# Kernel optimization log

Measured on AMD Instinct MI355X. Metric: run time of the kernel, lower is better.

The kernel has to match this reference:

```python
import jax, jax.numpy as jnp
import numpy as np

IN_SIZE = 171
HIDDEN = 1024
OUT_SIZE = 171
BATCH = 64
SEQ_LEN = 100
COND_NUM = 5
GT_NUM = 5


def _lstm_cell(x, h, c, w_ih, w_hh, b_ih, b_hh):
    # PyTorch LSTMCell: gates ordered (i, f, g, o)
    gates = x @ w_ih.T + h @ w_hh.T + b_ih + b_hh  # [B, 4H]
    i, f, g, o = jnp.split(gates, 4, axis=-1)
    i = jax.nn.sigmoid(i)
    f = jax.nn.sigmoid(f)
    g = jnp.tanh(g)
    o = jax.nn.sigmoid(o)
    c_new = f * c + i * g
    h_new = o * jnp.tanh(c_new)
    return h_new, c_new


def setup_inputs() -> dict:
    key = jax.random.key(0)
    ks = jax.random.split(key, 15)
    s = 1.0 / np.sqrt(HIDDEN)
    p = {}
    p["real_seq"] = jax.random.normal(ks[0], (BATCH, SEQ_LEN, IN_SIZE), dtype=jnp.float32)
    p["w_ih1"] = jax.random.uniform(ks[1], (4 * HIDDEN, IN_SIZE), minval=-s, maxval=s, dtype=jnp.float32)
    p["w_hh1"] = jax.random.uniform(ks[2], (4 * HIDDEN, HIDDEN), minval=-s, maxval=s, dtype=jnp.float32)
    p["b_ih1"] = jax.random.uniform(ks[3], (4 * HIDDEN,), minval=-s, maxval=s, dtype=jnp.float32)
    p["b_hh1"] = jax.random.uniform(ks[4], (4 * HIDDEN,), minval=-s, maxval=s, dtype=jnp.float32)
    p["w_ih2"] = jax.random.uniform(ks[5], (4 * HIDDEN, HIDDEN), minval=-s, maxval=s, dtype=jnp.float32)
    p["w_hh2"] = jax.random.uniform(ks[6], (4 * HIDDEN, HIDDEN), minval=-s, maxval=s, dtype=jnp.float32)
    p["b_ih2"] = jax.random.uniform(ks[7], (4 * HIDDEN,), minval=-s, maxval=s, dtype=jnp.float32)
    p["b_hh2"] = jax.random.uniform(ks[8], (4 * HIDDEN,), minval=-s, maxval=s, dtype=jnp.float32)
    p["w_ih3"] = jax.random.uniform(ks[9], (4 * HIDDEN, HIDDEN), minval=-s, maxval=s, dtype=jnp.float32)
    p["w_hh3"] = jax.random.uniform(ks[10], (4 * HIDDEN, HIDDEN), minval=-s, maxval=s, dtype=jnp.float32)
    p["b_ih3"] = jax.random.uniform(ks[11], (4 * HIDDEN,), minval=-s, maxval=s, dtype=jnp.float32)
    p["b_hh3"] = jax.random.uniform(ks[12], (4 * HIDDEN,), minval=-s, maxval=s, dtype=jnp.float32)
    p["dec_w"] = jax.random.uniform(ks[13], (OUT_SIZE, HIDDEN), minval=-s, maxval=s, dtype=jnp.float32)
    p["dec_b"] = jax.random.uniform(ks[14], (OUT_SIZE,), minval=-s, maxval=s, dtype=jnp.float32)
    return p


def _condition_lst(seq_len):
    gt = np.ones((100, GT_NUM))
    cond = np.zeros((100, COND_NUM))
    return np.concatenate((gt, cond), axis=1).reshape(-1)[:seq_len]


def reference(real_seq, w_ih1, w_hh1, b_ih1, b_hh1, w_ih2, w_hh2, b_ih2, b_hh2,
              w_ih3, w_hh3, b_ih3, b_hh3, dec_w, dec_b):
    batch, seq_len, _ = real_seq.shape
    cond = jnp.asarray(_condition_lst(seq_len), dtype=real_seq.dtype)  # [T], static pattern
    frames = jnp.swapaxes(real_seq, 0, 1)  # [T, B, in]
    z = jnp.zeros((batch, HIDDEN), dtype=real_seq.dtype)
    out0 = jnp.zeros((batch, OUT_SIZE), dtype=real_seq.dtype)

    def step(carry, xs):
        (h0, c0, h1, c1, h2, c2, prev_out) = carry
        frame, c = xs
        in_frame = jnp.where(c == 1, frame, prev_out)
        h0, c0 = _lstm_cell(in_frame, h0, c0, w_ih1, w_hh1, b_ih1, b_hh1)
        h1, c1 = _lstm_cell(h0, h1, c1, w_ih2, w_hh2, b_ih2, b_hh2)
        h2, c2 = _lstm_cell(h1, h2, c2, w_ih3, w_hh3, b_ih3, b_hh3)
        out = h2 @ dec_w.T + dec_b
        return (h0, c0, h1, c1, h2, c2, out), out

    _, outs = jax.lax.scan(step, (z, z, z, z, z, z, out0), (frames, cond))  # outs [T, B, out]
    # torch concatenates along dim=1 -> [B, T*out]
    return jnp.swapaxes(outs, 0, 1).reshape(batch, seq_len * OUT_SIZE)
```

## Files before the change

### kernel.cpp

```cpp
#include <hip/hip_runtime.h>
#include <hip/hip_fp16.h>


typedef unsigned short u16;
typedef unsigned int u32;
typedef _Float16 f16;
typedef _Float16 h8 __attribute__((ext_vector_type(8)));
typedef float f4 __attribute__((ext_vector_type(4)));

#define HSZ 65536

static __device__ __forceinline__ f4 mfma16(h8 a, h8 b, f4 c) {
  return __builtin_amdgcn_mfma_f32_16x16x32_f16(a, b, c, 0, 0, 0);
}

static __device__ __forceinline__ float fsig(float x) {
  return 1.f / (1.f + __expf(-x));
}
static __device__ __forceinline__ float ftanh(float x) {
  return 1.f - 2.f / (1.f + __expf(2.f * x));
}

struct P {
  const u16 *w1h, *weff, *w1x, *w2, *w3, *wdec, *fr;
  const float *br, *ba, *b2s, *b3s, *dec_b;
  u16 *h0, *h1, *h2;
  float* out;
  u32* bar;
};

template<int NJ>
static __device__ __forceinline__ void gemm_hreg(f4* acc, const u16* __restrict__ h,
                                                 const h8 (&wr)[NJ], int kq, int bt2,
                                                 int q, int c) {
#pragma unroll
  for (int jj = 0; jj < NJ; ++jj) {
    int kt = kq * 8 + jj;
    const u16* hp = h + (size_t)(kt * 4 + q) * 512;
    h8 b = wr[jj];
#pragma unroll
    for (int t = 0; t < 2; ++t) {
      h8 a = *(const h8*)(hp + ((bt2 * 2 + t) * 16 + c) * 8);
      acc[t] = mfma16(a, b, acc[t]);
    }
  }
}

static __device__ __forceinline__ void gemm_hlds(f4* acc, const u16* __restrict__ h,
                                                 const u16* lw, int ktbase, int kq,
                                                 int bt2, int q, int c, int lane) {
#pragma unroll
  for (int jj = 0; jj < 8; ++jj) {
    int kt = kq * 8 + jj;
    h8 b = *(const h8*)(lw + (size_t)((ktbase + kt) * 64 + lane) * 8);
    const u16* hp = h + (size_t)(kt * 4 + q) * 512;
#pragma unroll
    for (int t = 0; t < 2; ++t) {
      h8 a = *(const h8*)(hp + ((bt2 * 2 + t) * 16 + c) * 8);
      acc[t] = mfma16(a, b, acc[t]);
    }
  }
}

static __device__ __forceinline__ void gemm_fr(f4* acc, const u16* __restrict__ frt,
                                               const h8 (&wr)[2], int kq, int bt2,
                                               int q, int c) {
  if (kq < 3) {
#pragma unroll
    for (int jj = 0; jj < 2; ++jj) {
      int kt = kq * 2 + jj;
      h8 b = wr[jj];
#pragma unroll
      for (int t = 0; t < 2; ++t) {
        h8 a = *(const h8*)(frt + (size_t)((bt2 * 2 + t) * 16 + c) * 192 + kt * 32 + q * 8);
        acc[t] = mfma16(a, b, acc[t]);
      }
    }
  }
}

__launch_bounds__(512, 2)
__global__ void lstm_main(P p) {
  const int ng = blockIdx.x;
  const int tid = threadIdx.x;
  const int lane = tid & 63;
  const int w = tid >> 6;
  const int kq = w & 3;
  const int bt2 = w >> 2;
  const int c = lane & 15;
  const int q = lane >> 4;

  __shared__ u16 lds_w2[64 * 512];
  __shared__ u16 lds_w3[64 * 512];
  __shared__ float part[4 * 64 * 17];
  __shared__ float decp[8][64];

  {
    const uint4* s2 = (const uint4*)(p.w2 + (size_t)ng * 64 * 512);
    const uint4* s3 = (const uint4*)(p.w3 + (size_t)ng * 64 * 512);
    uint4* d2 = (uint4*)lds_w2;
    uint4* d3 = (uint4*)lds_w3;
    for (int i = tid; i < 4096; i += 512) { d2[i] = s2[i]; d3[i] = s3[i]; }
  }

  h8 r_w1h[8], r_weff[8], r_w1x[2];
  {
#pragma unroll
    for (int jj = 0; jj < 8; ++jj) {
      r_w1h[jj] = *(const h8*)(p.w1h + (size_t)((ng * 32 + kq * 8 + jj) * 64 + lane) * 8);
      r_weff[jj] = *(const h8*)(p.weff + (size_t)((ng * 32 + kq * 8 + jj) * 64 + lane) * 8);
    }
    if (kq < 3) {
#pragma unroll
      for (int jj = 0; jj < 2; ++jj)
        r_w1x[jj] = *(const h8*)(p.w1x + (size_t)((ng * 6 + kq * 2 + jj) * 64 + lane) * 8);
    }
  }

  float rb_r[16], rb_a[16], rb2[16], rb3[16];
  if (w == 0) {
#pragma unroll
    for (int i = 0; i < 16; ++i) {
      int idx = (i >> 2) * 1024 + ng * 4 + (i & 3);
      rb_r[i] = p.br[idx];  rb_a[i] = p.ba[idx];
      rb2[i] = p.b2s[idx];  rb3[i] = p.b3s[idx];
    }
  }
  const float dec_bng = (ng < 171) ? p.dec_b[ng] : 0.f;
  __syncthreads();

  float cr0[4] = {0, 0, 0, 0}, cr1[4] = {0, 0, 0, 0}, cr2[4] = {0, 0, 0, 0};
  u32 pub = 0;

  auto combine_pub = [&](float* crL, const float* rb, u16* hw) {
    u32 pk0 = 0, pk1 = 0;
#pragma unroll
    for (int u = 0; u < 4; ++u) {
      float s0 = rb[0 + u], s1 = rb[4 + u], s2 = rb[8 + u], s3 = rb[12 + u];
#pragma unroll
      for (int kqi = 0; kqi < 4; ++kqi) {
        const float* pp = &part[(kqi * 64 + lane) * 17 + u];
        s0 += pp[0]; s1 += pp[4]; s2 += pp[8]; s3 += pp[12];
      }
      float iv = fsig(s0), fv = fsig(s1), gv = ftanh(s2), ov = fsig(s3);
      float cn = fv * crL[u] + iv * gv;
      crL[u] = cn;
      f16 hh = (f16)(ov * ftanh(cn));
      u32 bits = (u32)*(const u16*)&hh;
      if (u < 2) pk0 |= bits << (16 * u); else pk1 |= bits << (16 * (u - 2));
    }
    u32* dst = (u32*)hw + (size_t)(ng >> 1) * 256 + lane * 4 + (ng & 1) * 2;
    __hip_atomic_store(dst, pk0, __ATOMIC_RELAXED, __HIP_MEMORY_SCOPE_AGENT);
    __hip_atomic_store(dst + 1, pk1, __ATOMIC_RELAXED, __HIP_MEMORY_SCOPE_AGENT);
    __builtin_amdgcn_s_waitcnt(0x0f70);
    if (lane == 0)
      __hip_atomic_store(p.bar + ng, pub, __ATOMIC_RELAXED, __HIP_MEMORY_SCOPE_AGENT);
  };

  auto waitall = [&]() {
    if (w == 0) {
      for (;;) {
        u32 v0 = __hip_atomic_load(p.bar + lane, __ATOMIC_RELAXED, __HIP_MEMORY_SCOPE_AGENT);
        u32 v1 = __hip_atomic_load(p.bar + 64 + lane, __ATOMIC_RELAXED, __HIP_MEMORY_SCOPE_AGENT);
        u32 v2 = __hip_atomic_load(p.bar + 128 + lane, __ATOMIC_RELAXED, __HIP_MEMORY_SCOPE_AGENT);
        u32 v3 = __hip_atomic_load(p.bar + 192 + lane, __ATOMIC_RELAXED, __HIP_MEMORY_SCOPE_AGENT);
        u32 m01 = v0 < v1 ? v0 : v1;
        u32 m23 = v2 < v3 ? v2 : v3;
        u32 mn = m01 < m23 ? m01 : m23;
        if (__all((int)(mn >= pub))) break;
      }
    }
    __syncthreads();
  };

  auto put_part = [&](const f4* acc) {
#pragma unroll
    for (int t = 0; t < 2; ++t)
#pragma unroll
      for (int r = 0; r < 4; ++r)
        part[(kq * 64 + bt2 * 32 + t * 16 + q * 4 + r) * 17 + c] = acc[t][r];
  };

  auto dec_partial = [&](const u16* __restrict__ h2b) {
    if (ng < 171) {
      const u16* hp = h2b + (size_t)w * 16 * 512 + lane * 8;
      const u16* wp = p.wdec + (size_t)ng * 1024 + w * 128;
      float s = 0.f;
#pragma unroll 4
      for (int i = 0; i < 16; ++i) {
        h8 hv = *(const h8*)(hp + (size_t)i * 512);
        h8 wv8 = *(const h8*)(wp + i * 8);
#pragma unroll
        for (int jj = 0; jj < 8; ++jj) s += (float)hv[jj] * (float)wv8[jj];
      }
      decp[w][lane] = s;
    }
  };
  auto dec_reduce = [&](int tout) {
    if (ng < 171) {
      float o = dec_bng;
#pragma unroll
      for (int i = 0; i < 8; ++i) o += decp[i][lane];
      p.out[(size_t)lane * 17100 + (size_t)tout * 171 + ng] = o;
    }
  };

  for (int t = 0; t < 100; ++t) {
    const bool cond = (t % 10) < 5;
    const u16* h0r = p.h0 + (size_t)t * HSZ;
    const u16* h1r = p.h1 + (size_t)t * HSZ;
    const u16* h2r = p.h2 + (size_t)t * HSZ;
    u16* h0w = p.h0 + (size_t)(t + 1) * HSZ;
    u16* h1w = p.h1 + (size_t)(t + 1) * HSZ;
    u16* h2w = p.h2 + (size_t)(t + 1) * HSZ;

    {
      f4 acc[2] = {{0, 0, 0, 0}, {0, 0, 0, 0}};
      gemm_hreg<8>(acc, h0r, r_w1h, kq, bt2, q, c);
      if (cond) {
        gemm_fr(acc, p.fr + (size_t)t * 64 * 192, r_w1x, kq, bt2, q, c);
        __syncthreads();
      } else {
        waitall();
        gemm_hreg<8>(acc, h2r, r_weff, kq, bt2, q, c);
      }
      put_part(acc);
      __syncthreads();
      ++pub;
      if (w == 0) combine_pub(cr0, cond ? rb_r : rb_a, h0w);
    }
    {
      f4 acc[2] = {{0, 0, 0, 0}, {0, 0, 0, 0}};
      gemm_hlds(acc, h1r, lds_w2, 32, kq, bt2, q, c, lane);
      waitall();
      gemm_hlds(acc, h0w, lds_w2, 0, kq, bt2, q, c, lane);
      put_part(acc);
      __syncthreads();
      ++pub;
      if (w == 0) combine_pub(cr1, rb2, h1w);
    }
    {
      f4 acc[2] = {{0, 0, 0, 0}, {0, 0, 0, 0}};
      gemm_hlds(acc, h2r, lds_w3, 32, kq, bt2, q, c, lane);
      if (t > 0) dec_partial(h2r);
      waitall();
      gemm_hlds(acc, h1w, lds_w3, 0, kq, bt2, q, c, lane);
      put_part(acc);
      __syncthreads();
      ++pub;
      if (w == 0) combine_pub(cr2, rb3, h2w);
      else if (w == 1 && t > 0) dec_reduce(t - 1);
    }
  }
  waitall();
  dec_partial(p.h2 + (size_t)100 * HSZ);
  __syncthreads();
  if (w == 0) dec_reduce(99);
}


__global__ void pack_w_kernel(const float* __restrict__ srcA, int KA,
                              const float* __restrict__ srcB, int KB,
                              u16* __restrict__ dst, int nkt) {
  int blk = blockIdx.x;
  int ng = blk / nkt, kt = blk % nkt;
  int lane = threadIdx.x;
  int c = lane & 15, q = lane >> 4;
  int row = (c >> 2) * 1024 + ng * 4 + (c & 3);
  int k0 = kt * 32 + q * 8;
  alignas(16) u16 outv[8];
  for (int j = 0; j < 8; ++j) {
    int k = k0 + j;
    float v = 0.f;
    if (k < KA) v = srcA[(size_t)row * KA + k];
    else if (k - KA < KB) v = srcB[(size_t)row * KB + (k - KA)];
    f16 hv = (f16)v;
    outv[j] = *(u16*)&hv;
  }
  *(uint4*)(dst + ((size_t)blk * 64 + lane) * 8) = *(const uint4*)outv;
}

__global__ void pack_weff_kernel(const float* __restrict__ w_ih1,
                                 const float* __restrict__ dec_w, u16* __restrict__ dst) {
  int blk = blockIdx.x;
  int ng = blk >> 5, kt = blk & 31;
  int lane = threadIdx.x;
  int c = lane & 15, q = lane >> 4;
  int row = (c >> 2) * 1024 + ng * 4 + (c & 3);
  int k0 = kt * 32 + q * 8;
  float acc[8] = {0.f, 0.f, 0.f, 0.f, 0.f, 0.f, 0.f, 0.f};
  for (int r = 0; r < 171; ++r) {
    float wi = w_ih1[(size_t)row * 171 + r];
    const float* dw = dec_w + (size_t)r * 1024 + k0;
#pragma unroll
    for (int j = 0; j < 8; ++j) acc[j] += wi * dw[j];
  }
  alignas(16) u16 outv[8];
  for (int j = 0; j < 8; ++j) { f16 hv = (f16)acc[j]; outv[j] = *(u16*)&hv; }
  *(uint4*)(dst + ((size_t)blk * 64 + lane) * 8) = *(const uint4*)outv;
}

__global__ void prep_bias_kernel(const float* b_ih1, const float* b_hh1,
                                 const float* w_ih1, const float* dec_b,
                                 const float* b_ih2, const float* b_hh2,
                                 const float* b_ih3, const float* b_hh3,
                                 float* br, float* ba, float* b2, float* b3) {
  int n = blockIdx.x * 256 + threadIdx.x;
  float s = b_ih1[n] + b_hh1[n];
  br[n] = s;
  float a = 0.f;
  for (int r = 0; r < 171; ++r) a += w_ih1[(size_t)n * 171 + r] * dec_b[r];
  ba[n] = s + a;
  b2[n] = b_ih2[n] + b_hh2[n];
  b3[n] = b_ih3[n] + b_hh3[n];
}

__global__ void pack_frames_kernel(const float* __restrict__ rs, u16* __restrict__ fr) {
  int i = blockIdx.x * 256 + threadIdx.x;
  int j = i % 192;
  int tb = i / 192;
  int b = tb % 64, t = tb / 64;
  float v = (j < 171) ? rs[((size_t)b * 100 + t) * 171 + j] : 0.f;
  f16 hv = (f16)v;
  fr[i] = *(u16*)&hv;
}

__global__ void pack_wdec_kernel(const float* __restrict__ dw, u16* __restrict__ dst) {
  int i = blockIdx.x * 256 + threadIdx.x;
  if (i < 171 * 1024) { f16 hv = (f16)dw[i]; dst[i] = *(u16*)&hv; }
}

__global__ void zero_kernel(u32* h0, u32* h1, u32* h2, u32* bar) {
  int i = blockIdx.x * 256 + threadIdx.x;
  h0[i] = 0; h1[i] = 0; h2[i] = 0;
  if (blockIdx.x < 8) bar[i] = 0;
}

extern "C" void kernel_launch(void* const* d_in, const int* in_sizes, int n_in,
                              void* d_out, int out_size, void* d_ws, size_t ws_size,
                              hipStream_t stream) {
  const float* real_seq = (const float*)d_in[0];
  const float* w_ih1 = (const float*)d_in[1];
  const float* w_hh1 = (const float*)d_in[2];
  const float* b_ih1 = (const float*)d_in[3];
  const float* b_hh1 = (const float*)d_in[4];
  const float* w_ih2 = (const float*)d_in[5];
  const float* w_hh2 = (const float*)d_in[6];
  const float* b_ih2 = (const float*)d_in[7];
  const float* b_hh2 = (const float*)d_in[8];
  const float* w_ih3 = (const float*)d_in[9];
  const float* w_hh3 = (const float*)d_in[10];
  const float* b_ih3 = (const float*)d_in[11];
  const float* b_hh3 = (const float*)d_in[12];
  const float* dec_w = (const float*)d_in[13];
  const float* dec_b = (const float*)d_in[14];

  char* ws = (char*)d_ws;
  size_t off = 0;
  auto alloc = [&](size_t bytes) {
    char* pp = ws + off;
    off += (bytes + 255) & ~(size_t)255;
    return pp;
  };
  u16* w1h  = (u16*)alloc(256ULL * 32 * 512 * 2);
  u16* weff = (u16*)alloc(256ULL * 32 * 512 * 2);
  u16* w1x  = (u16*)alloc(256ULL * 6 * 512 * 2);
  u16* w2   = (u16*)alloc(256ULL * 64 * 512 * 2);
  u16* w3   = (u16*)alloc(256ULL * 64 * 512 * 2);
  u16* wdec = (u16*)alloc(171ULL * 1024 * 2);
  u16* fr   = (u16*)alloc(100ULL * 64 * 192 * 2);
  u16* h0   = (u16*)alloc(101ULL * HSZ * 2);
  u16* h1   = (u16*)alloc(101ULL * HSZ * 2);
  u16* h2   = (u16*)alloc(101ULL * HSZ * 2);
  float* br  = (float*)alloc(4096 * 4);
  float* ba  = (float*)alloc(4096 * 4);
  float* b2s = (float*)alloc(4096 * 4);
  float* b3s = (float*)alloc(4096 * 4);
  u32* bar   = (u32*)alloc(8192);
  (void)ws_size; (void)in_sizes; (void)n_in; (void)out_size;

  pack_w_kernel<<<256 * 32, 64, 0, stream>>>(w_hh1, 1024, nullptr, 0, w1h, 32);
  pack_w_kernel<<<256 * 6, 64, 0, stream>>>(w_ih1, 171, nullptr, 0, w1x, 6);
  pack_w_kernel<<<256 * 64, 64, 0, stream>>>(w_ih2, 1024, w_hh2, 1024, w2, 64);
  pack_w_kernel<<<256 * 64, 64, 0, stream>>>(w_ih3, 1024, w_hh3, 1024, w3, 64);
  pack_weff_kernel<<<256 * 32, 64, 0, stream>>>(w_ih1, dec_w, weff);
  pack_wdec_kernel<<<(171 * 1024 + 255) / 256, 256, 0, stream>>>(dec_w, wdec);
  pack_frames_kernel<<<100 * 64 * 192 / 256, 256, 0, stream>>>(real_seq, fr);
  prep_bias_kernel<<<16, 256, 0, stream>>>(b_ih1, b_hh1, w_ih1, dec_b,
                                           b_ih2, b_hh2, b_ih3, b_hh3, br, ba, b2s, b3s);
  zero_kernel<<<128, 256, 0, stream>>>((u32*)h0, (u32*)h1, (u32*)h2, bar);

  P p{w1h, weff, w1x, w2, w3, wdec, fr, br, ba, b2s, b3s, dec_b,
      h0, h1, h2, (float*)d_out, bar};
  lstm_main<<<256, 512, 0, stream>>>(p);
}
```

Measured before the change: 2.031 ms.

## Swap MFMA operands so each lane owns full gate quartets, replace LDS reduction with flag handoff

Each MFMA now takes the weight tile as the A operand and hidden state as B, so every lane ends up with all four gates (i,f,g,o) for one hidden unit. The K dimension is split into two halves instead of four, and the two partial sums are combined through a per-wave LDS flag handoff instead of block-wide __syncthreads plus a single combining wave. Gate math is spread across four waves, and each block's arrival is counted with an LDS atomic before the global flag is published. This is meant to cut block-wide barriers and the serial single-wave combine on the recurrent critical path. In exchange it doubles the register-resident weights per wave, changes the hidden-state memory layout, and adds LDS spin-waits.

```diff
diff --git a/kernel.cpp b/kernel.cpp
--- a/kernel.cpp
+++ b/kernel.cpp
@@ -6,6 +6,7 @@
 typedef unsigned int u32;
 typedef _Float16 f16;
 typedef _Float16 h8 __attribute__((ext_vector_type(8)));
+typedef _Float16 h4 __attribute__((ext_vector_type(4)));
 typedef float f4 __attribute__((ext_vector_type(4)));
 
 #define HSZ 65536
@@ -13,7 +14,6 @@
 static __device__ __forceinline__ f4 mfma16(h8 a, h8 b, f4 c) {
   return __builtin_amdgcn_mfma_f32_16x16x32_f16(a, b, c, 0, 0, 0);
 }
-
 static __device__ __forceinline__ float fsig(float x) {
   return 1.f / (1.f + __expf(-x));
 }
@@ -29,53 +29,44 @@
   u32* bar;
 };
 
-template<int NJ>
-static __device__ __forceinline__ void gemm_hreg(f4* acc, const u16* __restrict__ h,
-                                                 const h8 (&wr)[NJ], int kq, int bt2,
+template<int NKT>
+static __device__ __forceinline__ void gemm_wreg(f4& acc, const u16* __restrict__ h,
+                                                 const h8* wr, int kh, int bt,
                                                  int q, int c) {
 #pragma unroll
-  for (int jj = 0; jj < NJ; ++jj) {
-    int kt = kq * 8 + jj;
-    const u16* hp = h + (size_t)(kt * 4 + q) * 512;
-    h8 b = wr[jj];
-#pragma unroll
-    for (int t = 0; t < 2; ++t) {
-      h8 a = *(const h8*)(hp + ((bt2 * 2 + t) * 16 + c) * 8);
-      acc[t] = mfma16(a, b, acc[t]);
-    }
-  }
-}
-
-static __device__ __forceinline__ void gemm_hlds(f4* acc, const u16* __restrict__ h,
-                                                 const u16* lw, int ktbase, int kq,
-                                                 int bt2, int q, int c, int lane) {
-#pragma unroll
-  for (int jj = 0; jj < 8; ++jj) {
-    int kt = kq * 8 + jj;
-    h8 b = *(const h8*)(lw + (size_t)((ktbase + kt) * 64 + lane) * 8);
-    const u16* hp = h + (size_t)(kt * 4 + q) * 512;
-#pragma unroll
-    for (int t = 0; t < 2; ++t) {
-      h8 a = *(const h8*)(hp + ((bt2 * 2 + t) * 16 + c) * 8);
-      acc[t] = mfma16(a, b, acc[t]);
-    }
-  }
-}
-
-static __device__ __forceinline__ void gemm_fr(f4* acc, const u16* __restrict__ frt,
-                                               const h8 (&wr)[2], int kq, int bt2,
-                                               int q, int c) {
-  if (kq < 3) {
-#pragma unroll
-    for (int jj = 0; jj < 2; ++jj) {
-      int kt = kq * 2 + jj;
-      h8 b = wr[jj];
-#pragma unroll
-      for (int t = 0; t < 2; ++t) {
-        h8 a = *(const h8*)(frt + (size_t)((bt2 * 2 + t) * 16 + c) * 192 + kt * 32 + q * 8);
-        acc[t] = mfma16(a, b, acc[t]);
-      }
-    }
+  for (int jj = 0; jj < NKT; ++jj) {
+    int kt = kh * 16 + jj;
+    const u16* hp = h + (size_t)(kt * 8 + 2 * q) * 256 + (bt * 16 + c) * 4;
+    h8 b;
+    *(h4*)&b = *(const h4*)hp;
+    *((h4*)&b + 1) = *(const h4*)(hp + 256);
+    acc = mfma16(wr[jj], b, acc);
+  }
+}
+
+static __device__ __forceinline__ void gemm_wlds(f4& acc, const u16* __restrict__ h,
+                                                 const u16* lw, int ktbase, int kh,
+                                                 int bt, int q, int c, int lane) {
+#pragma unroll
+  for (int jj = 0; jj < 16; ++jj) {
+    int kt = kh * 16 + jj;
+    h8 a = *(const h8*)(lw + (size_t)((ktbase + kt) * 64 + lane) * 8);
+    const u16* hp = h + (size_t)(kt * 8 + 2 * q) * 256 + (bt * 16 + c) * 4;
+    h8 b;
+    *(h4*)&b = *(const h4*)hp;
+    *((h4*)&b + 1) = *(const h4*)(hp + 256);
+    acc = mfma16(a, b, acc);
+  }
+}
+
+static __device__ __forceinline__ void gemm_fr(f4& acc, const u16* __restrict__ frt,
+                                               const u16* lwx, int bt, int q, int c,
+                                               int lane) {
+#pragma unroll
+  for (int kt = 0; kt < 6; ++kt) {
+    h8 a = *(const h8*)(lwx + (size_t)(kt * 64 + lane) * 8);
+    h8 b = *(const h8*)(frt + (size_t)(bt * 16 + c) * 192 + kt * 32 + q * 8);
+    acc = mfma16(a, b, acc);
   }
 }
 
@@ -85,77 +76,49 @@
   const int tid = threadIdx.x;
   const int lane = tid & 63;
   const int w = tid >> 6;
-  const int kq = w & 3;
-  const int bt2 = w >> 2;
+  const int kh = w & 1;
+  const int bt = w >> 1;
   const int c = lane & 15;
   const int q = lane >> 4;
 
   __shared__ u16 lds_w2[64 * 512];
   __shared__ u16 lds_w3[64 * 512];
-  __shared__ float part[4 * 64 * 17];
+  __shared__ u16 lds_w1x[6 * 512];
+  __shared__ f4 part[2][4][64];
+  __shared__ u32 flags[2][4];
+  __shared__ u32 arrv;
   __shared__ float decp[8][64];
 
   {
     const uint4* s2 = (const uint4*)(p.w2 + (size_t)ng * 64 * 512);
     const uint4* s3 = (const uint4*)(p.w3 + (size_t)ng * 64 * 512);
+    const uint4* sx = (const uint4*)(p.w1x + (size_t)ng * 6 * 512);
     uint4* d2 = (uint4*)lds_w2;
     uint4* d3 = (uint4*)lds_w3;
+    uint4* dx = (uint4*)lds_w1x;
     for (int i = tid; i < 4096; i += 512) { d2[i] = s2[i]; d3[i] = s3[i]; }
-  }
-
-  h8 r_w1h[8], r_weff[8], r_w1x[2];
-  {
-#pragma unroll
-    for (int jj = 0; jj < 8; ++jj) {
-      r_w1h[jj] = *(const h8*)(p.w1h + (size_t)((ng * 32 + kq * 8 + jj) * 64 + lane) * 8);
-      r_weff[jj] = *(const h8*)(p.weff + (size_t)((ng * 32 + kq * 8 + jj) * 64 + lane) * 8);
-    }
-    if (kq < 3) {
-#pragma unroll
-      for (int jj = 0; jj < 2; ++jj)
-        r_w1x[jj] = *(const h8*)(p.w1x + (size_t)((ng * 6 + kq * 2 + jj) * 64 + lane) * 8);
-    }
-  }
-
-  float rb_r[16], rb_a[16], rb2[16], rb3[16];
-  if (w == 0) {
-#pragma unroll
-    for (int i = 0; i < 16; ++i) {
-      int idx = (i >> 2) * 1024 + ng * 4 + (i & 3);
-      rb_r[i] = p.br[idx];  rb_a[i] = p.ba[idx];
-      rb2[i] = p.b2s[idx];  rb3[i] = p.b3s[idx];
-    }
+    if (tid < 384) dx[tid] = sx[tid];
+    if (tid == 0) { arrv = 0; flags[0][0] = flags[0][1] = flags[0][2] = flags[0][3] = 0;
+                    flags[1][0] = flags[1][1] = flags[1][2] = flags[1][3] = 0; }
+  }
+  h8 r_w1h[16], r_weff[16];
+#pragma unroll
+  for (int jj = 0; jj < 16; ++jj) {
+    r_w1h[jj] = *(const h8*)(p.w1h + (size_t)((ng * 32 + kh * 16 + jj) * 64 + lane) * 8);
+    r_weff[jj] = *(const h8*)(p.weff + (size_t)((ng * 32 + kh * 16 + jj) * 64 + lane) * 8);
+  }
+  float rb_r[4], rb_a[4], rb2[4], rb3[4];
+#pragma unroll
+  for (int r = 0; r < 4; ++r) {
+    int idx = r * 1024 + ng * 4 + q;
+    rb_r[r] = p.br[idx]; rb_a[r] = p.ba[idx];
+    rb2[r] = p.b2s[idx]; rb3[r] = p.b3s[idx];
   }
   const float dec_bng = (ng < 171) ? p.dec_b[ng] : 0.f;
   __syncthreads();
 
-  float cr0[4] = {0, 0, 0, 0}, cr1[4] = {0, 0, 0, 0}, cr2[4] = {0, 0, 0, 0};
+  float cr0 = 0.f, cr1 = 0.f, cr2 = 0.f;
   u32 pub = 0;
-
-  auto combine_pub = [&](float* crL, const float* rb, u16* hw) {
-    u32 pk0 = 0, pk1 = 0;
-#pragma unroll
-    for (int u = 0; u < 4; ++u) {
-      float s0 = rb[0 + u], s1 = rb[4 + u], s2 = rb[8 + u], s3 = rb[12 + u];
-#pragma unroll
-      for (int kqi = 0; kqi < 4; ++kqi) {
-        const float* pp = &part[(kqi * 64 + lane) * 17 + u];
-        s0 += pp[0]; s1 += pp[4]; s2 += pp[8]; s3 += pp[12];
-      }
-      float iv = fsig(s0), fv = fsig(s1), gv = ftanh(s2), ov = fsig(s3);
-      float cn = fv * crL[u] + iv * gv;
-      crL[u] = cn;
-      f16 hh = (f16)(ov * ftanh(cn));
-      u32 bits = (u32)*(const u16*)&hh;
-      if (u < 2) pk0 |= bits << (16 * u); else pk1 |= bits << (16 * (u - 2));
-    }
-    u32* dst = (u32*)hw + (size_t)(ng >> 1) * 256 + lane * 4 + (ng & 1) * 2;
-    __hip_atomic_store(dst, pk0, __ATOMIC_RELAXED, __HIP_MEMORY_SCOPE_AGENT);
-    __hip_atomic_store(dst + 1, pk1, __ATOMIC_RELAXED, __HIP_MEMORY_SCOPE_AGENT);
-    __builtin_amdgcn_s_waitcnt(0x0f70);
-    if (lane == 0)
-      __hip_atomic_store(p.bar + ng, pub, __ATOMIC_RELAXED, __HIP_MEMORY_SCOPE_AGENT);
-  };
 
   auto waitall = [&]() {
     if (w == 0) {
@@ -173,35 +136,55 @@
     __syncthreads();
   };
 
-  auto put_part = [&](const f4* acc) {
-#pragma unroll
-    for (int t = 0; t < 2; ++t)
-#pragma unroll
-      for (int r = 0; r < 4; ++r)
-        part[(kq * 64 + bt2 * 32 + t * 16 + q * 4 + r) * 17 + c] = acc[t][r];
+  auto finish = [&](f4 acc, float& cst, const float* rb, u16* hw) {
+    int par = pub & 1;
+    if (kh == 0) {
+      part[par][bt][lane] = acc;
+      __builtin_amdgcn_s_waitcnt(0xC07F);
+      if (lane == 0) *(volatile u32*)&flags[par][bt] = pub;
+    } else {
+      volatile u32* fp = &flags[par][bt];
+      while (*fp != pub) {}
+      f4 pt = part[par][bt][lane];
+      float s0 = acc[0] + pt[0] + rb[0];
+      float s1 = acc[1] + pt[1] + rb[1];
+      float s2 = acc[2] + pt[2] + rb[2];
+      float s3 = acc[3] + pt[3] + rb[3];
+      float iv = fsig(s0), fv = fsig(s1), gv = ftanh(s2), ov = fsig(s3);
+      float cn = fv * cst + iv * gv;
+      cst = cn;
+      f16 hh = (f16)(ov * ftanh(cn));
+      u32 bits = (u32)*(const u16*)&hh;
+      int srcA = ((lane & 1) * 2) * 16 + (lane >> 1);
+      u32 v0 = __shfl(bits, srcA, 64);
+      u32 v1 = __shfl(bits, srcA + 16, 64);
+      if (lane < 32) {
+        u32 pk = v0 | (v1 << 16);
+        u32* dst = (u32*)hw + (size_t)ng * 128 + bt * 32 + lane;
+        __hip_atomic_store(dst, pk, __ATOMIC_RELAXED, __HIP_MEMORY_SCOPE_AGENT);
+      }
+      __builtin_amdgcn_s_waitcnt(0x0F70);
+      if (lane == 0) {
+        u32 prev = atomicAdd(&arrv, 1u);
+        if (prev == pub * 4u - 1u)
+          __hip_atomic_store(p.bar + ng, pub, __ATOMIC_RELAXED, __HIP_MEMORY_SCOPE_AGENT);
+      }
+    }
   };
 
   auto dec_partial = [&](const u16* __restrict__ h2b) {
     if (ng < 171) {
-      const u16* hp = h2b + (size_t)w * 16 * 512 + lane * 8;
+      float s = 0.f;
+      const u16* hp = h2b + (size_t)w * 32 * 256 + lane * 4;
       const u16* wp = p.wdec + (size_t)ng * 1024 + w * 128;
-      float s = 0.f;
-#pragma unroll 4
-      for (int i = 0; i < 16; ++i) {
-        h8 hv = *(const h8*)(hp + (size_t)i * 512);
-        h8 wv8 = *(const h8*)(wp + i * 8);
-#pragma unroll
-        for (int jj = 0; jj < 8; ++jj) s += (float)hv[jj] * (float)wv8[jj];
+#pragma unroll 8
+      for (int i = 0; i < 32; ++i) {
+        h4 hv = *(const h4*)(hp + (size_t)i * 256);
+        h4 wv = *(const h4*)(wp + i * 4);
+#pragma unroll
+        for (int jj = 0; jj < 4; ++jj) s += (float)hv[jj] * (float)wv[jj];
       }
       decp[w][lane] = s;
-    }
-  };
-  auto dec_reduce = [&](int tout) {
-    if (ng < 171) {
-      float o = dec_bng;
-#pragma unroll
-      for (int i = 0; i < 8; ++i) o += decp[i][lane];
-      p.out[(size_t)lane * 17100 + (size_t)tout * 171 + ng] = o;
     }
   };
 
@@ -215,47 +198,55 @@
     u16* h2w = p.h2 + (size_t)(t + 1) * HSZ;
 
     {
-      f4 acc[2] = {{0, 0, 0, 0}, {0, 0, 0, 0}};
-      gemm_hreg<8>(acc, h0r, r_w1h, kq, bt2, q, c);
+      f4 acc = {0, 0, 0, 0};
+      gemm_wreg<16>(acc, h0r, r_w1h, kh, bt, q, c);
       if (cond) {
-        gemm_fr(acc, p.fr + (size_t)t * 64 * 192, r_w1x, kq, bt2, q, c);
-        __syncthreads();
+        if (kh == 0) gemm_fr(acc, p.fr + (size_t)t * 64 * 192, lds_w1x, bt, q, c, lane);
       } else {
         waitall();
-        gemm_hreg<8>(acc, h2r, r_weff, kq, bt2, q, c);
-      }
-      put_part(acc);
-      __syncthreads();
+        gemm_wreg<16>(acc, h2r, r_weff, kh, bt, q, c);
+      }
       ++pub;
-      if (w == 0) combine_pub(cr0, cond ? rb_r : rb_a, h0w);
+      finish(acc, cr0, cond ? rb_r : rb_a, h0w);
     }
     {
-      f4 acc[2] = {{0, 0, 0, 0}, {0, 0, 0, 0}};
-      gemm_hlds(acc, h1r, lds_w2, 32, kq, bt2, q, c, lane);
-      waitall();
-      gemm_hlds(acc, h0w, lds_w2, 0, kq, bt2, q, c, lane);
-      put_part(acc);
-      __syncthreads();
+      f4 acc = {0, 0, 0, 0};
+      if (cond) {
+        waitall();
+        gemm_wlds(acc, h1r, lds_w2, 32, kh, bt, q, c, lane);
+      } else {
+        gemm_wlds(acc, h1r, lds_w2, 32, kh, bt, q, c, lane);
+        waitall();
+      }
+      gemm_wlds(acc, h0w, lds_w2, 0, kh, bt, q, c, lane);
       ++pub;
-      if (w == 0) combine_pub(cr1, rb2, h1w);
+      finish(acc, cr1, rb2, h1w);
     }
     {
-      f4 acc[2] = {{0, 0, 0, 0}, {0, 0, 0, 0}};
-      gemm_hlds(acc, h2r, lds_w3, 32, kq, bt2, q, c, lane);
+      f4 acc = {0, 0, 0, 0};
+      gemm_wlds(acc, h2r, lds_w3, 32, kh, bt, q, c, lane);
       if (t > 0) dec_partial(h2r);
       waitall();
-      gemm_hlds(acc, h1w, lds_w3, 0, kq, bt2, q, c, lane);
-      put_part(acc);
-      __syncthreads();
+      gemm_wlds(acc, h1w, lds_w3, 0, kh, bt, q, c, lane);
+      if (w == 2 && t > 0 && ng < 171) {
+        float o = dec_bng;
+#pragma unroll
+        for (int i = 0; i < 8; ++i) o += decp[i][lane];
+        p.out[(size_t)lane * 17100 + (size_t)(t - 1) * 171 + ng] = o;
+      }
       ++pub;
-      if (w == 0) combine_pub(cr2, rb3, h2w);
-      else if (w == 1 && t > 0) dec_reduce(t - 1);
+      finish(acc, cr2, rb3, h2w);
     }
   }
   waitall();
   dec_partial(p.h2 + (size_t)100 * HSZ);
   __syncthreads();
-  if (w == 0) dec_reduce(99);
+  if (w == 0 && ng < 171) {
+    float o = dec_bng;
+#pragma unroll
+    for (int i = 0; i < 8; ++i) o += decp[i][lane];
+    p.out[(size_t)lane * 17100 + (size_t)99 * 171 + ng] = o;
+  }
 }
 
 
@@ -265,17 +256,29 @@
   int blk = blockIdx.x;
   int ng = blk / nkt, kt = blk % nkt;
   int lane = threadIdx.x;
-  int c = lane & 15, q = lane >> 4;
-  int row = (c >> 2) * 1024 + ng * 4 + (c & 3);
-  int k0 = kt * 32 + q * 8;
+  int c = lane & 15, qq = lane >> 4;
+  int row = (c & 3) * 1024 + ng * 4 + (c >> 2);
+  int k0 = kt * 32 + qq * 8;
   alignas(16) u16 outv[8];
-  for (int j = 0; j < 8; ++j) {
-    int k = k0 + j;
-    float v = 0.f;
-    if (k < KA) v = srcA[(size_t)row * KA + k];
-    else if (k - KA < KB) v = srcB[(size_t)row * KB + (k - KA)];
-    f16 hv = (f16)v;
-    outv[j] = *(u16*)&hv;
+  if (k0 + 8 <= KA) {
+    const float4* s = (const float4*)(srcA + (size_t)row * KA + k0);
+    float4 a = s[0], b = s[1];
+    float vv[8] = {a.x, a.y, a.z, a.w, b.x, b.y, b.z, b.w};
+    for (int j = 0; j < 8; ++j) { f16 hv = (f16)vv[j]; outv[j] = *(u16*)&hv; }
+  } else if (k0 >= KA && k0 + 8 <= KA + KB) {
+    const float4* s = (const float4*)(srcB + (size_t)row * KB + (k0 - KA));
+    float4 a = s[0], b = s[1];
+    float vv[8] = {a.x, a.y, a.z, a.w, b.x, b.y, b.z, b.w};
+    for (int j = 0; j < 8; ++j) { f16 hv = (f16)vv[j]; outv[j] = *(u16*)&hv; }
+  } else {
+    for (int j = 0; j < 8; ++j) {
+      int k = k0 + j;
+      float v = 0.f;
+      if (k < KA) v = srcA[(size_t)row * KA + k];
+      else if (k - KA < KB) v = srcB[(size_t)row * KB + (k - KA)];
+      f16 hv = (f16)v;
+      outv[j] = *(u16*)&hv;
+    }
   }
   *(uint4*)(dst + ((size_t)blk * 64 + lane) * 8) = *(const uint4*)outv;
 }
@@ -285,9 +288,9 @@
   int blk = blockIdx.x;
   int ng = blk >> 5, kt = blk & 31;
   int lane = threadIdx.x;
-  int c = lane & 15, q = lane >> 4;
-  int row = (c >> 2) * 1024 + ng * 4 + (c & 3);
-  int k0 = kt * 32 + q * 8;
+  int c = lane & 15, qq = lane >> 4;
+  int row = (c & 3) * 1024 + ng * 4 + (c >> 2);
+  int k0 = kt * 32 + qq * 8;
   float acc[8] = {0.f, 0.f, 0.f, 0.f, 0.f, 0.f, 0.f, 0.f};
   for (int r = 0; r < 171; ++r) {
     float wi = w_ih1[(size_t)row * 171 + r];
```

New measurement: 2.970 ms. 1.46x slower.
